# Kernel tuning notes

Hardware: AMD Instinct MI355X
Metric: run time of the kernel (lower is better)

Reference implementation:

```python
import jax, jax.numpy as jnp
from jax import lax
import numpy as np

HIDDEN_DIM = 64
INPUT_DIM = 1
NUM_CLASSES = 3
B, T = 2048, 512


def _lstm_layer(x_tbd, w_ih, w_hh, b_ih, b_hh):
    # x_tbd: [T, B, D_in]; PyTorch gate order: i, f, g, o
    H = w_hh.shape[1]
    bsz = x_tbd.shape[1]
    # precompute input projections for all timesteps: [T, B, 4H]
    xp = jnp.einsum('tbd,gd->tbg', x_tbd, w_ih) + b_ih + b_hh

    def step(carry, xg):
        h, c = carry
        gates = xg + h @ w_hh.T  # [B, 4H]
        i, f, g, o = jnp.split(gates, 4, axis=-1)
        i = jax.nn.sigmoid(i)
        f = jax.nn.sigmoid(f)
        g = jnp.tanh(g)
        o = jax.nn.sigmoid(o)
        c = f * c + i * g
        h = o * jnp.tanh(c)
        return (h, c), h

    h0 = jnp.zeros((bsz, H), dtype=x_tbd.dtype)
    c0 = jnp.zeros((bsz, H), dtype=x_tbd.dtype)
    (h_last, _), ys = lax.scan(step, (h0, c0), xp)
    return ys, h_last


def setup_inputs() -> dict:
    key = jax.random.key(0)
    ks = jax.random.split(key, 12)
    s_in = 1.0 / np.sqrt(HIDDEN_DIM)
    H4 = 4 * HIDDEN_DIM
    return {
        'x': jax.random.normal(ks[0], (B, T, INPUT_DIM), dtype=jnp.float32),
        'w_ih0': jax.random.uniform(ks[1], (H4, INPUT_DIM), minval=-s_in, maxval=s_in),
        'w_hh0': jax.random.uniform(ks[2], (H4, HIDDEN_DIM), minval=-s_in, maxval=s_in),
        'b_ih0': jax.random.uniform(ks[3], (H4,), minval=-s_in, maxval=s_in),
        'b_hh0': jax.random.uniform(ks[4], (H4,), minval=-s_in, maxval=s_in),
        'w_ih1': jax.random.uniform(ks[5], (H4, HIDDEN_DIM), minval=-s_in, maxval=s_in),
        'w_hh1': jax.random.uniform(ks[6], (H4, HIDDEN_DIM), minval=-s_in, maxval=s_in),
        'b_ih1': jax.random.uniform(ks[7], (H4,), minval=-s_in, maxval=s_in),
        'b_hh1': jax.random.uniform(ks[8], (H4,), minval=-s_in, maxval=s_in),
        'w_fc': jax.random.uniform(ks[9], (NUM_CLASSES, HIDDEN_DIM), minval=-s_in, maxval=s_in),
        'b_fc': jax.random.uniform(ks[10], (NUM_CLASSES,), minval=-s_in, maxval=s_in),
    }


def reference(x, w_ih0, w_hh0, b_ih0, b_hh0, w_ih1, w_hh1, b_ih1, b_hh1, w_fc, b_fc):
    # eval-mode forward (dropout between layers disabled)
    x_tbd = jnp.transpose(x, (1, 0, 2))  # [T, B, 1]
    ys0, _ = _lstm_layer(x_tbd, w_ih0, w_hh0, b_ih0, b_hh0)  # [T, B, H]
    _, h_last = _lstm_layer(ys0, w_ih1, w_hh1, b_ih1, b_hh1)  # [B, H]
    return h_last @ w_fc.T + b_fc  # [B, NUM_CLASSES]
```

## Files before the change

### kernel.cpp

```cpp
#include <hip/hip_runtime.h>


typedef _Float16 half8    __attribute__((ext_vector_type(8)));
typedef float    float4_t __attribute__((ext_vector_type(4)));
typedef float    float2v  __attribute__((ext_vector_type(2)));

#define T_STEPS 512
#define SIG_K  (-1.442695040888963f)
#define TANH_K (-2.885390081777927f)

__device__ __forceinline__ int hoff(int slot, int row, int kb, int lo) {
    return slot * 1024 + row * 64 + (((kb + row) & 7) << 3) + lo;
}

__device__ __forceinline__ float2v lstm_cell2(float2v zi, float2v zf,
                                              float2v zg, float2v zo,
                                              float2v& c) {
    float2v ei, ef, vv, eo;
    ei[0] = __builtin_amdgcn_exp2f(zi[0]); ei[1] = __builtin_amdgcn_exp2f(zi[1]);
    ef[0] = __builtin_amdgcn_exp2f(zf[0]); ef[1] = __builtin_amdgcn_exp2f(zf[1]);
    vv[0] = __builtin_amdgcn_exp2f(zg[0]); vv[1] = __builtin_amdgcn_exp2f(zg[1]);
    eo[0] = __builtin_amdgcn_exp2f(zo[0]); eo[1] = __builtin_amdgcn_exp2f(zo[1]);
    const float2v one = {1.f, 1.f};
    const float2v pi = one + ei, pf = one + ef, pv = one + vv, po = one + eo;
    const float2v A   = pi * pv;
    const float2v num = c * A + (one - vv) * pf;
    const float2v d   = pf * A;
    float2v rd;
    rd[0] = __builtin_amdgcn_rcpf(d[0]); rd[1] = __builtin_amdgcn_rcpf(d[1]);
    const float2v cn = num * rd;
    c = cn;
    const float2v ct = cn * TANH_K;
    float2v u;
    u[0] = __builtin_amdgcn_exp2f(ct[0]); u[1] = __builtin_amdgcn_exp2f(ct[1]);
    const float2v den = po * (one + u);
    float2v rn;
    rn[0] = __builtin_amdgcn_rcpf(den[0]); rn[1] = __builtin_amdgcn_rcpf(den[1]);
    return (one - u) * rn;
}

extern "C" __global__ __launch_bounds__(512, 1)
void lstm2_mfma(const float* __restrict__ x,
                const float* __restrict__ w_ih0, const float* __restrict__ w_hh0,
                const float* __restrict__ b_ih0, const float* __restrict__ b_hh0,
                const float* __restrict__ w_ih1, const float* __restrict__ w_hh1,
                const float* __restrict__ b_ih1, const float* __restrict__ b_hh1,
                const float* __restrict__ w_fc,  const float* __restrict__ b_fc,
                float* __restrict__ out)
{
    __shared__ float    x_lds[T_STEPS][8];
    __shared__ _Float16 bufA[2 * 1024];
    __shared__ _Float16 bufB[2 * 1024];
    __shared__ float    hfin[8][68];

    const int tid  = threadIdx.x;
    const int wv   = tid >> 6;
    const int lane = tid & 63;
    const int cr   = lane & 15;
    const int kg   = lane >> 4;
    const int rb   = kg * 4;
    const int b0   = blockIdx.x * 8;
    const bool isL0 = (wv < 4);
    const int u    = wv & 3;
    const int ucol = u * 16 + cr;
    const int wkb  = 2 * u + (cr >> 3);

    for (int idx = tid; idx < 8 * T_STEPS; idx += 512) {
        const int r = idx >> 9, t = idx & (T_STEPS - 1);
        x_lds[t][r] = x[(long)(b0 + r) * T_STEPS + t];
    }
    for (int idx = tid; idx < 2 * 1024; idx += 512) {
        bufA[idx] = (_Float16)0.f;
        bufB[idx] = (_Float16)0.f;
    }

    half8 wf[4][4];
    float4_t bias4[4];
    float2v  wi0b[4];
    #pragma unroll
    for (int g = 0; g < 4; ++g) {
        const float sc = (g == 2) ? TANH_K : SIG_K;
        const int col = g * 64 + ucol;
        if (isL0) {
            const float b = (b_ih0[col] + b_hh0[col]) * sc;
            bias4[g] = (float4_t){b, b, b, b};
            const float w = w_ih0[col] * sc;
            wi0b[g] = (float2v){w, w};
            #pragma unroll
            for (int kt = 0; kt < 2; ++kt) {
                const float* src = w_hh0 + col * 64 + kt * 32 + kg * 8;
                #pragma unroll
                for (int i = 0; i < 8; ++i) wf[g][kt][i] = (_Float16)(src[i] * sc);
            }
        } else {
            const float b = (b_ih1[col] + b_hh1[col]) * sc;
            bias4[g] = (float4_t){b, b, b, b};
            wi0b[g] = (float2v){0.f, 0.f};
            #pragma unroll
            for (int kt = 0; kt < 4; ++kt) {
                const int k0 = kt * 32 + kg * 8;
                const float* src = (k0 < 64) ? (w_ih1 + col * 64 + k0)
                                             : (w_hh1 + col * 64 + (k0 - 64));
                #pragma unroll
                for (int i = 0; i < 8; ++i) wf[g][kt][i] = (_Float16)(src[i] * sc);
            }
        }
    }

    const int rd0s0 = hoff(0, cr, kg,     0), rd0s1 = hoff(1, cr, kg,     0);
    const int rd1s0 = hoff(0, cr, 4 + kg, 0), rd1s1 = hoff(1, cr, 4 + kg, 0);
    const int w0s0  = hoff(0, rb,     wkb, cr & 7);
    const int w1s0  = hoff(0, rb + 1, wkb, cr & 7);
    const int w0s1  = hoff(1, rb,     wkb, cr & 7);
    const int w1s1  = hoff(1, rb + 1, wkb, cr & 7);

    float2v cc2 = {0.f, 0.f};
    float2v hv2 = {0.f, 0.f};

    auto l0_step = [&](int kk, int rd0, int rd1, int wo0, int wo1)
        __attribute__((always_inline)) {
        const half8 a0 = *(const half8*)&bufA[rd0];
        const half8 a1 = *(const half8*)&bufA[rd1];
        float4_t acc[4];
        #pragma unroll
        for (int g = 0; g < 4; ++g) {
            acc[g] = __builtin_amdgcn_mfma_f32_16x16x32_f16(a0, wf[g][0], bias4[g], 0, 0, 0);
            acc[g] = __builtin_amdgcn_mfma_f32_16x16x32_f16(a1, wf[g][1], acc[g], 0, 0, 0);
        }
        const float2v xq = *(const float2v*)&x_lds[kk][2 * kg];
        float2v z[4];
        #pragma unroll
        for (int g = 0; g < 4; ++g) {
            const float2v ap = {acc[g][0], acc[g][1]};
            z[g] = xq * wi0b[g] + ap;
        }
        const float2v h = lstm_cell2(z[0], z[1], z[2], z[3], cc2);
        bufA[wo0] = (_Float16)h[0];
        bufA[wo1] = (_Float16)h[1];
    };
    auto l1_step = [&](int rd0, int rd1, int rB0, int rB1, int wo0, int wo1)
        __attribute__((always_inline)) {
        const half8 a0  = *(const half8*)&bufA[rd0];
        const half8 a1  = *(const half8*)&bufA[rd1];
        const half8 bh0 = *(const half8*)&bufB[rB0];
        const half8 bh1 = *(const half8*)&bufB[rB1];
        float4_t acc[4];
        #pragma unroll
        for (int g = 0; g < 4; ++g) {
            acc[g] = __builtin_amdgcn_mfma_f32_16x16x32_f16(a0,  wf[g][0], bias4[g], 0, 0, 0);
            acc[g] = __builtin_amdgcn_mfma_f32_16x16x32_f16(a1,  wf[g][1], acc[g], 0, 0, 0);
            acc[g] = __builtin_amdgcn_mfma_f32_16x16x32_f16(bh0, wf[g][2], acc[g], 0, 0, 0);
            acc[g] = __builtin_amdgcn_mfma_f32_16x16x32_f16(bh1, wf[g][3], acc[g], 0, 0, 0);
        }
        float2v z[4];
        #pragma unroll
        for (int g = 0; g < 4; ++g)
            z[g] = (float2v){acc[g][0], acc[g][1]};
        hv2 = lstm_cell2(z[0], z[1], z[2], z[3], cc2);
        bufB[wo0] = (_Float16)hv2[0];
        bufB[wo1] = (_Float16)hv2[1];
    };

    __syncthreads();

    if (isL0) l0_step(0, rd0s1, rd1s1, w0s0, w1s0);
    __syncthreads();

    for (int k = 1; k <= 509; k += 2) {
        if (isL0) l0_step(k, rd0s0, rd1s0, w0s1, w1s1);
        else      l1_step(rd0s0, rd1s0, rd0s1, rd1s1, w0s0, w1s0);
        __syncthreads();
        if (isL0) l0_step(k + 1, rd0s1, rd1s1, w0s0, w1s0);
        else      l1_step(rd0s1, rd1s1, rd0s0, rd1s0, w0s1, w1s1);
        __syncthreads();
    }

    if (isL0) l0_step(511, rd0s0, rd1s0, w0s1, w1s1);
    else      l1_step(rd0s0, rd1s0, rd0s1, rd1s1, w0s0, w1s0);
    __syncthreads();
    if (!isL0) l1_step(rd0s1, rd1s1, rd0s0, rd1s0, w0s1, w1s1);
    __syncthreads();

    if (!isL0) {
        hfin[2 * kg + 0][ucol] = hv2[0];
        hfin[2 * kg + 1][ucol] = hv2[1];
    }
    __syncthreads();

    if (tid < 24) {
        const int row = tid / 3, cls = tid - row * 3;
        float s = b_fc[cls];
        const float* wr = w_fc + cls * 64;
        #pragma unroll 8
        for (int uu = 0; uu < 64; ++uu) s += hfin[row][uu] * wr[uu];
        out[(long)(b0 + row) * 3 + cls] = s;
    }
}

extern "C" void kernel_launch(void* const* d_in, const int* in_sizes, int n_in,
                              void* d_out, int out_size, void* d_ws, size_t ws_size,
                              hipStream_t stream) {
    const float* xx     = (const float*)d_in[0];
    const float* w_ih0  = (const float*)d_in[1];
    const float* w_hh0  = (const float*)d_in[2];
    const float* b_ih0  = (const float*)d_in[3];
    const float* b_hh0  = (const float*)d_in[4];
    const float* w_ih1  = (const float*)d_in[5];
    const float* w_hh1  = (const float*)d_in[6];
    const float* b_ih1  = (const float*)d_in[7];
    const float* b_hh1  = (const float*)d_in[8];
    const float* w_fc   = (const float*)d_in[9];
    const float* b_fc   = (const float*)d_in[10];
    float* out = (float*)d_out;

    lstm2_mfma<<<dim3(256), dim3(512), 0, stream>>>(
        xx, w_ih0, w_hh0, b_ih0, b_hh0,
        w_ih1, w_hh1, b_ih1, b_hh1, w_fc, b_fc, out);
}
```

Measured before the change: 219.2 us.

## Split LSTM steps into MFMA and cell phases, interleaving layer waves

Each layer's timestep is split into an MFMA phase and an elementwise cell phase separated by barriers. The schedule offsets the two layers so that layer-0 waves run MFMAs while layer-1 waves run transcendental cell math, and the reverse. The aim is to overlap matrix-core work with VALU/transcendental work across the wave groups instead of having both layers do the same kind of work at once. The cost is twice as many block-wide barriers per timestep, and accumulators must now stay live across a barrier.

```diff
diff --git a/kernel.cpp b/kernel.cpp
--- a/kernel.cpp
+++ b/kernel.cpp
@@ -116,46 +116,50 @@
 
     float2v cc2 = {0.f, 0.f};
     float2v hv2 = {0.f, 0.f};
-
-    auto l0_step = [&](int kk, int rd0, int rd1, int wo0, int wo1)
-        __attribute__((always_inline)) {
+    float4_t acc0[4];
+    float4_t acc1[4];
+    #pragma unroll
+    for (int g = 0; g < 4; ++g) { acc0[g] = bias4[g]; acc1[g] = bias4[g]; }
+
+    auto l0_mfma = [&](int rd0, int rd1) __attribute__((always_inline)) {
         const half8 a0 = *(const half8*)&bufA[rd0];
         const half8 a1 = *(const half8*)&bufA[rd1];
-        float4_t acc[4];
         #pragma unroll
         for (int g = 0; g < 4; ++g) {
-            acc[g] = __builtin_amdgcn_mfma_f32_16x16x32_f16(a0, wf[g][0], bias4[g], 0, 0, 0);
-            acc[g] = __builtin_amdgcn_mfma_f32_16x16x32_f16(a1, wf[g][1], acc[g], 0, 0, 0);
-        }
+            acc0[g] = __builtin_amdgcn_mfma_f32_16x16x32_f16(a0, wf[g][0], bias4[g], 0, 0, 0);
+            acc0[g] = __builtin_amdgcn_mfma_f32_16x16x32_f16(a1, wf[g][1], acc0[g], 0, 0, 0);
+        }
+    };
+    auto l0_epi = [&](int kk, int wo0, int wo1) __attribute__((always_inline)) {
         const float2v xq = *(const float2v*)&x_lds[kk][2 * kg];
         float2v z[4];
         #pragma unroll
         for (int g = 0; g < 4; ++g) {
-            const float2v ap = {acc[g][0], acc[g][1]};
+            const float2v ap = {acc0[g][0], acc0[g][1]};
             z[g] = xq * wi0b[g] + ap;
         }
         const float2v h = lstm_cell2(z[0], z[1], z[2], z[3], cc2);
         bufA[wo0] = (_Float16)h[0];
         bufA[wo1] = (_Float16)h[1];
     };
-    auto l1_step = [&](int rd0, int rd1, int rB0, int rB1, int wo0, int wo1)
-        __attribute__((always_inline)) {
+    auto l1_mfma = [&](int rd0, int rd1, int rB0, int rB1) __attribute__((always_inline)) {
         const half8 a0  = *(const half8*)&bufA[rd0];
         const half8 a1  = *(const half8*)&bufA[rd1];
         const half8 bh0 = *(const half8*)&bufB[rB0];
         const half8 bh1 = *(const half8*)&bufB[rB1];
-        float4_t acc[4];
         #pragma unroll
         for (int g = 0; g < 4; ++g) {
-            acc[g] = __builtin_amdgcn_mfma_f32_16x16x32_f16(a0,  wf[g][0], bias4[g], 0, 0, 0);
-            acc[g] = __builtin_amdgcn_mfma_f32_16x16x32_f16(a1,  wf[g][1], acc[g], 0, 0, 0);
-            acc[g] = __builtin_amdgcn_mfma_f32_16x16x32_f16(bh0, wf[g][2], acc[g], 0, 0, 0);
-            acc[g] = __builtin_amdgcn_mfma_f32_16x16x32_f16(bh1, wf[g][3], acc[g], 0, 0, 0);
-        }
+            acc1[g] = __builtin_amdgcn_mfma_f32_16x16x32_f16(a0,  wf[g][0], bias4[g], 0, 0, 0);
+            acc1[g] = __builtin_amdgcn_mfma_f32_16x16x32_f16(a1,  wf[g][1], acc1[g], 0, 0, 0);
+            acc1[g] = __builtin_amdgcn_mfma_f32_16x16x32_f16(bh0, wf[g][2], acc1[g], 0, 0, 0);
+            acc1[g] = __builtin_amdgcn_mfma_f32_16x16x32_f16(bh1, wf[g][3], acc1[g], 0, 0, 0);
+        }
+    };
+    auto l1_epi = [&](int wo0, int wo1) __attribute__((always_inline)) {
         float2v z[4];
         #pragma unroll
         for (int g = 0; g < 4; ++g)
-            z[g] = (float2v){acc[g][0], acc[g][1]};
+            z[g] = (float2v){acc1[g][0], acc1[g][1]};
         hv2 = lstm_cell2(z[0], z[1], z[2], z[3], cc2);
         bufB[wo0] = (_Float16)hv2[0];
         bufB[wo1] = (_Float16)hv2[1];
@@ -163,22 +167,37 @@
 
     __syncthreads();
 
-    if (isL0) l0_step(0, rd0s1, rd1s1, w0s0, w1s0);
-    __syncthreads();
-
-    for (int k = 1; k <= 509; k += 2) {
-        if (isL0) l0_step(k, rd0s0, rd1s0, w0s1, w1s1);
-        else      l1_step(rd0s0, rd1s0, rd0s1, rd1s1, w0s0, w1s0);
-        __syncthreads();
-        if (isL0) l0_step(k + 1, rd0s1, rd1s1, w0s0, w1s0);
-        else      l1_step(rd0s1, rd1s1, rd0s0, rd1s0, w0s1, w1s1);
-        __syncthreads();
-    }
-
-    if (isL0) l0_step(511, rd0s0, rd1s0, w0s1, w1s1);
-    else      l1_step(rd0s0, rd1s0, rd0s1, rd1s1, w0s0, w1s0);
-    __syncthreads();
-    if (!isL0) l1_step(rd0s1, rd1s1, rd0s0, rd1s0, w0s1, w1s1);
+    if (isL0) l0_mfma(rd0s1, rd1s1);
+    __syncthreads();
+    if (isL0) l0_epi(0, w0s0, w1s0);
+    __syncthreads();
+
+    if (isL0) l0_mfma(rd0s0, rd1s0);
+    __syncthreads();
+    if (isL0) l0_epi(1, w0s1, w1s1);
+    else      l1_mfma(rd0s0, rd1s0, rd0s1, rd1s1);
+    __syncthreads();
+
+    for (int k = 2; k <= 510; k += 2) {
+        if (isL0) l0_mfma(rd0s1, rd1s1);
+        else      l1_epi(w0s0, w1s0);
+        __syncthreads();
+        if (isL0) l0_epi(k, w0s0, w1s0);
+        else      l1_mfma(rd0s1, rd1s1, rd0s0, rd1s0);
+        __syncthreads();
+        if (isL0) l0_mfma(rd0s0, rd1s0);
+        else      l1_epi(w0s1, w1s1);
+        __syncthreads();
+        if (isL0) l0_epi(k + 1, w0s1, w1s1);
+        else      l1_mfma(rd0s0, rd1s0, rd0s1, rd1s1);
+        __syncthreads();
+    }
+
+    if (!isL0) l1_epi(w0s0, w1s0);
+    __syncthreads();
+    if (!isL0) l1_mfma(rd0s1, rd1s1, rd0s0, rd1s0);
+    __syncthreads();
+    if (!isL0) l1_epi(w0s1, w1s1);
     __syncthreads();
 
     if (!isL0) {
```

Result: slower. 280.0 us (+27.7%).
